# Optimization experiments

Hardware: AMD Instinct MI355X
Metric: run time of the kernel (lower is better)

Reference implementation:

```python
import jax, jax.numpy as jnp
import numpy as np

N_BINS = 15


def setup_inputs() -> dict:
    key = jax.random.key(0)
    k1, k2 = jax.random.split(key)
    N, C = 2097152, 50
    logits = jax.random.normal(k1, (N, C), dtype=jnp.float32)
    labels = jax.random.randint(k2, (N,), 0, C, dtype=jnp.int64)
    return {"logits": logits, "labels": labels}


def reference(logits, labels):
    n = logits.shape[0]
    probs = jax.nn.softmax(logits, axis=1)
    confidences = jnp.max(probs, axis=1)                 # [N]
    predictions = jnp.argmax(probs, axis=1)              # [N]
    accuracies = (predictions == labels).astype(jnp.float32)

    # bin i covers (i/n_bins, (i+1)/n_bins]; searchsorted(left) on the upper
    # boundaries gives the first upper >= conf, matching conf.gt(lo)*conf.le(hi)
    uppers = jnp.linspace(0.0, 1.0, N_BINS + 1)[1:]
    bin_id = jnp.clip(jnp.searchsorted(uppers, confidences, side="left"), 0, N_BINS - 1)

    ones = jnp.ones_like(confidences)
    counts = jax.ops.segment_sum(ones, bin_id, num_segments=N_BINS)
    sum_acc = jax.ops.segment_sum(accuracies, bin_id, num_segments=N_BINS)
    sum_conf = jax.ops.segment_sum(confidences, bin_id, num_segments=N_BINS)

    prop_in_bin = counts / n
    nonempty = counts > 0
    denom = jnp.maximum(counts, 1.0)
    avg_acc = sum_acc / denom
    avg_conf = sum_conf / denom

    gap = avg_conf - avg_acc
    bin_over_confidence = jnp.where(nonempty, gap * prop_in_bin, 0.0)   # [n_bins]
    ece = jnp.sum(jnp.where(nonempty, jnp.abs(gap) * prop_in_bin, 0.0)).reshape(1)
    return (ece, bin_over_confidence, prop_in_bin)
```

## Files before the change

### kernel.cpp

```cpp
#include <hip/hip_runtime.h>
#include <math.h>

#define N_BINS 15
#define C 50
#define ROWS_PER_TILE 64
#define TILE_FLOATS (ROWS_PER_TILE * C)
#define WAVES_PER_BLOCK 4
#define BLOCK (WAVES_PER_BLOCK * 64)
#define GRID 768


__device__ __forceinline__ void load_lds16(const float* g, float* l) {
    __builtin_amdgcn_global_load_lds(
        (const __attribute__((address_space(1))) unsigned int*)g,
        (__attribute__((address_space(3))) unsigned int*)l, 16, 0, 0);
}

__global__ __launch_bounds__(BLOCK) void ece_accum(
    const float* __restrict__ logits,
    const int*   __restrict__ labels,
    unsigned int* __restrict__ ws_cnt,
    unsigned int* __restrict__ ws_acc,
    float*        __restrict__ ws_conf,
    int n_rows)
{
    __shared__ float tiles[WAVES_PER_BLOCK * TILE_FLOATS];
    __shared__ unsigned int s_cnt[N_BINS];
    __shared__ unsigned int s_acc[N_BINS];
    __shared__ float        s_conf[N_BINS];

    const int tid = threadIdx.x;
    if (tid < N_BINS) { s_cnt[tid] = 0u; s_acc[tid] = 0u; s_conf[tid] = 0.0f; }
    __syncthreads();

    const int wave = tid >> 6;
    const int lane = tid & 63;
    float* __restrict__ wtile = &tiles[wave * TILE_FLOATS];

    const int n_tiles  = n_rows / ROWS_PER_TILE;
    const int gwave    = blockIdx.x * WAVES_PER_BLOCK + wave;
    const int n_gwaves = GRID * WAVES_PER_BLOCK;

    for (int t = gwave; t < n_tiles; t += n_gwaves) {
        const float* __restrict__ src = logits + (size_t)t * TILE_FLOATS;

        asm volatile("s_waitcnt lgkmcnt(0)" ::: "memory");

        #pragma unroll
        for (int j = 0; j < 12; ++j)
            load_lds16(src + (j * 64 + lane) * 4, wtile + j * 256);
        if (lane < 32)
            load_lds16(src + (12 * 64 + lane) * 4, wtile + 12 * 256);

        int label = labels[t * ROWS_PER_TILE + lane];

        asm volatile("s_waitcnt vmcnt(0)" ::: "memory");

        const float2* __restrict__ r2 = (const float2*)(wtile + lane * C);
        float vals[C];
        #pragma unroll
        for (int k = 0; k < C / 2; ++k) {
            float2 p = r2[k];
            vals[2 * k]     = p.x;
            vals[2 * k + 1] = p.y;
        }

        float vmax = vals[0];
        int   amax = 0;
        #pragma unroll
        for (int k = 1; k < C; ++k)
            if (vals[k] > vmax) { vmax = vals[k]; amax = k; }

        float sum = 0.0f;
        #pragma unroll
        for (int k = 0; k < C; ++k) sum += __expf(vals[k] - vmax);
        float conf = 1.0f / sum;

        int bin = (int)ceilf(conf * 15.0f) - 1;
        bin = bin < 0 ? 0 : (bin > N_BINS - 1 ? N_BINS - 1 : bin);

        atomicAdd(&s_cnt[bin], 1u);
        if (amax == label) atomicAdd(&s_acc[bin], 1u);
        atomicAdd(&s_conf[bin], conf);
    }

    const int rem_start = n_tiles * ROWS_PER_TILE;
    const int rem = n_rows - rem_start;
    if (blockIdx.x == 0 && tid < rem) {
        const float* __restrict__ r = logits + (size_t)(rem_start + tid) * C;
        float vmax = r[0];
        int   amax = 0;
        for (int k = 1; k < C; ++k) {
            float v = r[k];
            if (v > vmax) { vmax = v; amax = k; }
        }
        float sum = 0.0f;
        for (int k = 0; k < C; ++k) sum += __expf(r[k] - vmax);
        float conf = 1.0f / sum;
        int bin = (int)ceilf(conf * 15.0f) - 1;
        bin = bin < 0 ? 0 : (bin > N_BINS - 1 ? N_BINS - 1 : bin);
        atomicAdd(&s_cnt[bin], 1u);
        if (amax == labels[rem_start + tid]) atomicAdd(&s_acc[bin], 1u);
        atomicAdd(&s_conf[bin], conf);
    }

    __syncthreads();
    if (tid < N_BINS && s_cnt[tid] != 0u) {
        atomicAdd(&ws_cnt[tid],  s_cnt[tid]);
        atomicAdd(&ws_acc[tid],  s_acc[tid]);
        atomicAdd(&ws_conf[tid], s_conf[tid]);
    }
}

__global__ __launch_bounds__(64) void ece_final(
    const unsigned int* __restrict__ ws_cnt,
    const unsigned int* __restrict__ ws_acc,
    const float*        __restrict__ ws_conf,
    float* __restrict__ out, float inv_n)
{
    int i = threadIdx.x;
    float v = 0.0f;
    if (i < N_BINS) {
        float cnt      = (float)ws_cnt[i];
        float prop     = cnt * inv_n;
        float denom    = fmaxf(cnt, 1.0f);
        float avg_acc  = (float)ws_acc[i] / denom;
        float avg_conf = ws_conf[i] / denom;
        float gap      = avg_conf - avg_acc;
        bool  nonempty = cnt > 0.0f;
        out[1 + i]  = nonempty ? gap * prop : 0.0f;
        out[16 + i] = prop;
        v = nonempty ? fabsf(gap) * prop : 0.0f;
    }
    v += __shfl_down(v, 8, 64);
    v += __shfl_down(v, 4, 64);
    v += __shfl_down(v, 2, 64);
    v += __shfl_down(v, 1, 64);
    if (i == 0) out[0] = v;
}

extern "C" void kernel_launch(void* const* d_in, const int* in_sizes, int n_in,
                              void* d_out, int out_size, void* d_ws, size_t ws_size,
                              hipStream_t stream)
{
    const float* logits = (const float*)d_in[0];
    const int*   labels = (const int*)d_in[1];
    const int n_rows = in_sizes[1];

    unsigned int* ws_cnt  = (unsigned int*)d_ws;
    unsigned int* ws_acc  = ws_cnt + N_BINS;
    float*        ws_conf = (float*)(ws_acc + N_BINS);

    hipMemsetAsync(d_ws, 0, 3 * N_BINS * sizeof(float), stream);

    ece_accum<<<GRID, BLOCK, 0, stream>>>(logits, labels, ws_cnt, ws_acc, ws_conf, n_rows);
    ece_final<<<1, 64, 0, stream>>>(ws_cnt, ws_acc, ws_conf, (float*)d_out,
                                    1.0f / (float)n_rows);
}
```

Baseline: 549.9 us.

## Double-buffer LDS tile staging and replace per-row shared atomics with register bins

Each wave now keeps two LDS tile buffers and prefetches the next tile (and its labels) before computing the current one, waiting only on the older loads via a partial vmcnt. Per-row LDS atomics are replaced by per-lane register histograms, with count and accuracy packed into one 32-bit value. These are reduced by wave shuffles and flushed once per wave at the end. Waves per block drop from 4 to 2 to keep LDS use the same. The risks are higher register pressure from the 30 accumulators and a 16-bit packing overflow if one lane sees more than 65535 rows in a bin, which cannot happen at this size.

```diff
diff --git a/kernel.cpp b/kernel.cpp
--- a/kernel.cpp
+++ b/kernel.cpp
@@ -5,15 +5,25 @@
 #define C 50
 #define ROWS_PER_TILE 64
 #define TILE_FLOATS (ROWS_PER_TILE * C)
-#define WAVES_PER_BLOCK 4
+#define WAVES_PER_BLOCK 2
 #define BLOCK (WAVES_PER_BLOCK * 64)
 #define GRID 768
+#define N_GWAVES (GRID * WAVES_PER_BLOCK)
 
 
 __device__ __forceinline__ void load_lds16(const float* g, float* l) {
     __builtin_amdgcn_global_load_lds(
         (const __attribute__((address_space(1))) unsigned int*)g,
         (__attribute__((address_space(3))) unsigned int*)l, 16, 0, 0);
+}
+
+__device__ __forceinline__ void stage_tile(const float* __restrict__ src,
+                                           float* __restrict__ dst, int lane) {
+    #pragma unroll
+    for (int j = 0; j < 12; ++j)
+        load_lds16(src + (j * 64 + lane) * 4, dst + j * 256);
+    if (lane < 32)
+        load_lds16(src + (12 * 64 + lane) * 4, dst + 12 * 256);
 }
 
 __global__ __launch_bounds__(BLOCK) void ece_accum(
@@ -24,7 +34,7 @@
     float*        __restrict__ ws_conf,
     int n_rows)
 {
-    __shared__ float tiles[WAVES_PER_BLOCK * TILE_FLOATS];
+    __shared__ float tiles[WAVES_PER_BLOCK][2][TILE_FLOATS];
     __shared__ unsigned int s_cnt[N_BINS];
     __shared__ unsigned int s_acc[N_BINS];
     __shared__ float        s_conf[N_BINS];
@@ -35,28 +45,37 @@
 
     const int wave = tid >> 6;
     const int lane = tid & 63;
-    float* __restrict__ wtile = &tiles[wave * TILE_FLOATS];
-
-    const int n_tiles  = n_rows / ROWS_PER_TILE;
-    const int gwave    = blockIdx.x * WAVES_PER_BLOCK + wave;
-    const int n_gwaves = GRID * WAVES_PER_BLOCK;
-
-    for (int t = gwave; t < n_tiles; t += n_gwaves) {
-        const float* __restrict__ src = logits + (size_t)t * TILE_FLOATS;
-
-        asm volatile("s_waitcnt lgkmcnt(0)" ::: "memory");
-
-        #pragma unroll
-        for (int j = 0; j < 12; ++j)
-            load_lds16(src + (j * 64 + lane) * 4, wtile + j * 256);
-        if (lane < 32)
-            load_lds16(src + (12 * 64 + lane) * 4, wtile + 12 * 256);
-
-        int label = labels[t * ROWS_PER_TILE + lane];
-
-        asm volatile("s_waitcnt vmcnt(0)" ::: "memory");
-
-        const float2* __restrict__ r2 = (const float2*)(wtile + lane * C);
+
+    unsigned int ca[N_BINS];
+    float        cs[N_BINS];
+    #pragma unroll
+    for (int b = 0; b < N_BINS; ++b) { ca[b] = 0u; cs[b] = 0.0f; }
+
+    const int n_tiles = n_rows / ROWS_PER_TILE;
+    int t      = blockIdx.x * WAVES_PER_BLOCK + wave;
+    int parity = 0;
+    int lbl    = 0;
+
+    if (t < n_tiles) {
+        stage_tile(logits + (size_t)t * TILE_FLOATS, &tiles[wave][0][0], lane);
+        lbl = labels[t * ROWS_PER_TILE + lane];
+    }
+
+    while (t < n_tiles) {
+        const int nxt = t + N_GWAVES;
+        int lbl_nxt = 0;
+        if (nxt < n_tiles) {
+            asm volatile("s_waitcnt lgkmcnt(0)" ::: "memory");
+            stage_tile(logits + (size_t)nxt * TILE_FLOATS,
+                       &tiles[wave][parity ^ 1][0], lane);
+            lbl_nxt = labels[nxt * ROWS_PER_TILE + lane];
+            asm volatile("s_waitcnt vmcnt(14)" ::: "memory");
+        } else {
+            asm volatile("s_waitcnt vmcnt(0)" ::: "memory");
+        }
+
+        const float2* __restrict__ r2 =
+            (const float2*)(&tiles[wave][parity][0] + lane * C);
         float vals[C];
         #pragma unroll
         for (int k = 0; k < C / 2; ++k) {
@@ -79,9 +98,33 @@
         int bin = (int)ceilf(conf * 15.0f) - 1;
         bin = bin < 0 ? 0 : (bin > N_BINS - 1 ? N_BINS - 1 : bin);
 
-        atomicAdd(&s_cnt[bin], 1u);
-        if (amax == label) atomicAdd(&s_acc[bin], 1u);
-        atomicAdd(&s_conf[bin], conf);
+        const unsigned int inc = (amax == lbl) ? 0x10001u : 1u;
+        #pragma unroll
+        for (int b = 0; b < N_BINS; ++b) {
+            const bool h = (bin == b);
+            ca[b] += h ? inc : 0u;
+            cs[b] += h ? conf : 0.0f;
+        }
+
+        lbl = lbl_nxt;
+        parity ^= 1;
+        t = nxt;
+    }
+
+    #pragma unroll
+    for (int b = 0; b < N_BINS; ++b) {
+        unsigned int c = ca[b];
+        float        f = cs[b];
+        #pragma unroll
+        for (int off = 32; off > 0; off >>= 1) {
+            c += (unsigned int)__shfl_xor((int)c, off, 64);
+            f += __shfl_xor(f, off, 64);
+        }
+        if (lane == 0) {
+            atomicAdd(&s_cnt[b], c & 0xFFFFu);
+            atomicAdd(&s_acc[b], c >> 16);
+            atomicAdd(&s_conf[b], f);
+        }
     }
 
     const int rem_start = n_tiles * ROWS_PER_TILE;
```

Result: no change. 559.3 us (+1.7%).
